# Performance work log

Hardware: AMD Instinct MI355X
Metric: run time of the kernel (lower is better)

The kernel has to match this reference:

```python
import jax, jax.numpy as jnp
import numpy as np

C, U, V, D, B = 5, 6144, 6144, 64, 4096  # classes, users, items, feat dim, batch pairs


def setup_inputs() -> dict:
    key = jax.random.key(0)
    ks = jax.random.split(key, 16)
    s = 1.0 / np.sqrt(D)
    adj = (jax.random.uniform(ks[0], (C, U, V)) < 0.01).astype(jnp.float32)
    return {
        "u": jax.random.randint(ks[1], (B,), 0, U),
        "v": jax.random.randint(ks[2], (B,), 0, V),
        "u_emb": jax.random.normal(ks[3], (U, D), jnp.float32) * 0.1,
        "v_emb": jax.random.normal(ks[4], (V, D), jnp.float32) * 0.1,
        "W1u": jax.random.normal(ks[5], (C, D, D), jnp.float32) * s,
        "b1u": jnp.zeros((C, D), jnp.float32),
        "W1v": jax.random.normal(ks[6], (C, D, D), jnp.float32) * s,
        "b1v": jnp.zeros((C, D), jnp.float32),
        "W2u": jax.random.normal(ks[7], (C, D, D), jnp.float32) * s,
        "b2u": jnp.zeros((C, D), jnp.float32),
        "W2v": jax.random.normal(ks[8], (C, D, D), jnp.float32) * s,
        "b2v": jnp.zeros((C, D), jnp.float32),
        "Q": jax.random.normal(ks[9], (C, D, D), jnp.float32) * s,
        "adj": adj,
    }


def reference(u, v, u_emb, v_emb, W1u, b1u, W1v, b1v, W2u, b2u, W2v, b2v, Q, adj):
    # ---- layer 1: per-class graph convolution, summed over rating classes ----
    # user codes aggregate item features through adj_c; item codes through adj_c^T
    msg_v = jnp.einsum("vd,cde->cve", v_emb, W1v)            # [C,V,D]
    h_u = jax.nn.relu(jnp.einsum("cuv,cve->ue", adj, msg_v) + b1v.sum(0))  # [U,D]
    msg_u = jnp.einsum("ud,cde->cue", u_emb, W1u)            # [C,U,D]
    h_v = jax.nn.relu(jnp.einsum("cuv,cue->ve", adj, msg_u) + b1u.sum(0))  # [V,D]
    # ---- layer 2 ----
    z_u = jnp.einsum("cuv,cve->ue", adj, jnp.einsum("vd,cde->cve", h_v, W2u)) + b2u.sum(0)
    z_v = jnp.einsum("cuv,cue->ve", adj, jnp.einsum("ud,cde->cue", h_u, W2v)) + b2v.sum(0)
    # ---- bilinear decoder over batch of (user, item) pairs ----
    zu = z_u[u]                                              # [B,D] gather
    zv = z_v[v]                                              # [B,D] gather
    logits = jnp.einsum("bd,cde,be->bc", zu, Q, zv)          # [B,C] per-class rating logits
    return logits
```

## Files before the change

kernel.cpp:

```cpp
#include <hip/hip_runtime.h>

#define NC   5
#define NU   6144
#define NV   6144
#define ND   64
#define NB   4096
#define CAP  128
#define HALF (NC * NU)

__device__ __forceinline__ unsigned int spread4(unsigned int x) {
  x &= 0xFFu;
  x = (x | (x << 12)) & 0x000F000Fu;
  x = (x | (x << 6))  & 0x03030303u;
  x = (x | (x << 3))  & 0x11111111u;
  return x;
}

__global__ __launch_bounds__(256) void k_adj2idx(
    const float* __restrict__ adj,
    int* __restrict__ cnt,
    unsigned short* __restrict__ idx) {
  __shared__ unsigned int rowwords[64][9];
  const int x = blockIdx.x & 7;
  const int s = blockIdx.x >> 3;
  const int tv = s % 24;
  const int S = (s / 24) * 8 + x;
  const int c  = S / 96;
  const int tu = S - c * 96;
  const int wave = threadIdx.x >> 6;
  const int lane = threadIdx.x & 63;

  float4 av[16];
  {
    const float* base = adj +
        ((size_t)(c * NU + tu * 64 + wave * 16) * NV + tv * 256);
    #pragma unroll
    for (int rr = 0; rr < 16; ++rr)
      av[rr] = ((const float4*)(base + (size_t)rr * NV))[lane];
  }
  #pragma unroll
  for (int rr = 0; rr < 16; ++rr) {
    const unsigned long long b0 = __ballot(av[rr].x != 0.0f);
    const unsigned long long b1 = __ballot(av[rr].y != 0.0f);
    const unsigned long long b2 = __ballot(av[rr].z != 0.0f);
    const unsigned long long b3 = __ballot(av[rr].w != 0.0f);
    if (lane < 8) {
      const unsigned int e0 = spread4((unsigned int)(b0 >> (lane * 8)));
      const unsigned int e1 = spread4((unsigned int)(b1 >> (lane * 8)));
      const unsigned int e2 = spread4((unsigned int)(b2 >> (lane * 8)));
      const unsigned int e3 = spread4((unsigned int)(b3 >> (lane * 8)));
      rowwords[wave * 16 + rr][lane] = e0 | (e1 << 1) | (e2 << 2) | (e3 << 3);
    }
  }
  __syncthreads();

  #pragma unroll
  for (int p = 0; p < 2; ++p) {
    const int rloc = lane >> 3;
    const int wloc = lane & 7;
    const int r = wave * 16 + p * 8 + rloc;
    const unsigned int wbits = rowwords[r][wloc];
    const int pc = __popc(wbits);
    int pre = pc;
    #pragma unroll
    for (int d = 1; d < 8; d <<= 1) {
      const int y = __shfl_up(pre, d, 64);
      if (wloc >= d) pre += y;
    }
    const int total = __shfl(pre, rloc * 8 + 7, 64);
    const int excl  = pre - pc;
    const int R = c * 6144 + tu * 64 + r;
    int base = 0;
    if (wloc == 0 && total > 0) base = atomicAdd(&cnt[R], total);
    base = __shfl(base, rloc * 8, 64);
    unsigned int m = wbits;
    int o = base + excl;
    unsigned short* orow = idx + (size_t)R * CAP;
    const int vbase = tv * 256 + wloc * 32;
    while (m) {
      const int bb = __ffs(m) - 1;
      if (o < CAP) orow[o] = (unsigned short)(vbase + bb);
      ++o;
      m &= m - 1;
    }
  }

  {
    const int j = threadIdx.x;
    const int w = j >> 5, bit = j & 31;
    unsigned int w0 = 0, w1 = 0;
    #pragma unroll
    for (int r = 0; r < 32; ++r) {
      w0 |= ((rowwords[r][w]      >> bit) & 1u) << r;
      w1 |= ((rowwords[r + 32][w] >> bit) & 1u) << r;
    }
    const int cj = __popc(w0) + __popc(w1);
    if (cj > 0) {
      const int R = (NC + c) * 6144 + tv * 256 + j;
      int o = atomicAdd(&cnt[R], cj);
      unsigned short* orow = idx + (size_t)R * CAP;
      const int ubase = tu * 64;
      unsigned int m = w0;
      while (m) {
        const int bb = __ffs(m) - 1;
        if (o < CAP) orow[o] = (unsigned short)(ubase + bb);
        ++o;
        m &= m - 1;
      }
      m = w1;
      while (m) {
        const int bb = __ffs(m) - 1;
        if (o < CAP) orow[o] = (unsigned short)(ubase + 32 + bb);
        ++o;
        m &= m - 1;
      }
    }
  }
}

__global__ __launch_bounds__(256) void k_layer(
    const int* __restrict__ cnt,
    const unsigned short* __restrict__ idx,
    const float* __restrict__ tabA,
    const float* __restrict__ tabB,
    const float* __restrict__ Wa, const float* __restrict__ ba,
    float* __restrict__ outA,
    const float* __restrict__ Wb, const float* __restrict__ bb,
    float* __restrict__ outB,
    int do_relu) {
  __shared__ float4 lds_agg[NC][16][16];
  const int side = blockIdx.x >= 384;
  const int r0   = (blockIdx.x - side * 384) * 16;
  const float4* tab = (const float4*)(side ? tabB : tabA);
  const float* W    = side ? Wb : Wa;
  const float* bias = side ? bb : ba;
  float* out        = side ? outB : outA;
  const int wave = threadIdx.x >> 6;
  const int lane = threadIdx.x & 63;
  const int g    = lane >> 4;
  const int e16  = lane & 15;

  for (int rr = wave * 4; rr < wave * 4 + 4; ++rr) {
    for (int c = 0; c < NC; ++c) {
      const int R = side * HALF + c * 6144 + r0 + rr;
      int n = cnt[R];
      n = n > CAP ? CAP : n;
      const unsigned short* l = idx + (size_t)R * CAP;
      float4 a0 = make_float4(0.f,0.f,0.f,0.f), a1 = a0, a2 = a0, a3 = a0;
      int i = 0;
      for (; i + 16 <= n; i += 16) {
        const int j0 = l[i + g], j1 = l[i + 4 + g];
        const int j2 = l[i + 8 + g], j3 = l[i + 12 + g];
        const float4 x0 = tab[j0 * 16 + e16];
        const float4 x1 = tab[j1 * 16 + e16];
        const float4 x2 = tab[j2 * 16 + e16];
        const float4 x3 = tab[j3 * 16 + e16];
        a0.x += x0.x; a0.y += x0.y; a0.z += x0.z; a0.w += x0.w;
        a1.x += x1.x; a1.y += x1.y; a1.z += x1.z; a1.w += x1.w;
        a2.x += x2.x; a2.y += x2.y; a2.z += x2.z; a2.w += x2.w;
        a3.x += x3.x; a3.y += x3.y; a3.z += x3.z; a3.w += x3.w;
      }
      for (; i + 4 <= n; i += 4) {
        const float4 x = tab[(int)l[i + g] * 16 + e16];
        a0.x += x.x; a0.y += x.y; a0.z += x.z; a0.w += x.w;
      }
      if (i + g < n) {
        const float4 x = tab[(int)l[i + g] * 16 + e16];
        a1.x += x.x; a1.y += x.y; a1.z += x.z; a1.w += x.w;
      }
      a0.x += a1.x + a2.x + a3.x;
      a0.y += a1.y + a2.y + a3.y;
      a0.z += a1.z + a2.z + a3.z;
      a0.w += a1.w + a2.w + a3.w;
      #pragma unroll
      for (int off = 16; off < 64; off <<= 1) {
        a0.x += __shfl_xor(a0.x, off, 64);
        a0.y += __shfl_xor(a0.y, off, 64);
        a0.z += __shfl_xor(a0.z, off, 64);
        a0.w += __shfl_xor(a0.w, off, 64);
      }
      if (g == 0) lds_agg[c][rr][e16] = a0;
    }
  }
  __syncthreads();

  float bs = 0.0f;
  #pragma unroll
  for (int c = 0; c < NC; ++c) bs += bias[c * 64 + lane];
  float acc[4] = {bs, bs, bs, bs};
  for (int c = 0; c < NC; ++c) {
    float w[64];
    #pragma unroll
    for (int d = 0; d < 64; ++d) w[d] = W[c * 4096 + d * 64 + lane];
    #pragma unroll
    for (int r = 0; r < 4; ++r) {
      #pragma unroll
      for (int d4 = 0; d4 < 16; ++d4) {
        const float4 a = lds_agg[c][wave * 4 + r][d4];
        acc[r] = fmaf(a.x, w[d4 * 4 + 0], acc[r]);
        acc[r] = fmaf(a.y, w[d4 * 4 + 1], acc[r]);
        acc[r] = fmaf(a.z, w[d4 * 4 + 2], acc[r]);
        acc[r] = fmaf(a.w, w[d4 * 4 + 3], acc[r]);
      }
    }
  }
  #pragma unroll
  for (int r = 0; r < 4; ++r) {
    const float v = do_relu ? fmaxf(acc[r], 0.0f) : acc[r];
    out[(size_t)(r0 + wave * 4 + r) * 64 + lane] = v;
  }
}

__global__ __launch_bounds__(256) void k_decoder(
    const int* __restrict__ uu, const int* __restrict__ vv,
    const float* __restrict__ z_u, const float* __restrict__ z_v,
    const float* __restrict__ Q,
    float* __restrict__ out) {
  const int lane = threadIdx.x & 63;
  const int wave = threadIdx.x >> 6;
  const int b = blockIdx.x * 4 + wave;
  const int ub = uu[b];
  const int vb = vv[b];
  const float zve = z_v[(size_t)vb * 64 + lane];
  const float* zu = z_u + (size_t)ub * 64;
  #pragma unroll
  for (int c = 0; c < NC; ++c) {
    const float* Qc = Q + c * 64 * 64;
    float t = 0.0f;
    #pragma unroll
    for (int d = 0; d < 64; ++d) t = fmaf(zu[d], Qc[d * 64 + lane], t);
    float p = t * zve;
    #pragma unroll
    for (int off = 32; off > 0; off >>= 1) p += __shfl_xor(p, off, 64);
    if (lane == 0) out[(size_t)b * NC + c] = p;
  }
}

extern "C" void kernel_launch(void* const* d_in, const int* in_sizes, int n_in,
                              void* d_out, int out_size, void* d_ws, size_t ws_size,
                              hipStream_t stream) {
  const int*   u     = (const int*)d_in[0];
  const int*   v     = (const int*)d_in[1];
  const float* u_emb = (const float*)d_in[2];
  const float* v_emb = (const float*)d_in[3];
  const float* W1u   = (const float*)d_in[4];
  const float* b1u   = (const float*)d_in[5];
  const float* W1v   = (const float*)d_in[6];
  const float* b1v   = (const float*)d_in[7];
  const float* W2u   = (const float*)d_in[8];
  const float* b2u   = (const float*)d_in[9];
  const float* W2v   = (const float*)d_in[10];
  const float* b2v   = (const float*)d_in[11];
  const float* Q     = (const float*)d_in[12];
  const float* adj   = (const float*)d_in[13];
  float* out = (float*)d_out;

  char* ws = (char*)d_ws;
  int* cnt = (int*)ws;
  unsigned short* idxL = (unsigned short*)(ws + 245760);
  char* fbase = ws + 245760 + 15728640;
  float* h_u = (float*)fbase;
  float* h_v = (float*)(fbase + 1572864);
  float* z_u = (float*)(fbase + 3145728);
  float* z_v = (float*)(fbase + 4718592);

  hipMemsetAsync(cnt, 0, 2 * NC * 6144 * sizeof(int), stream);

  k_adj2idx<<<NC * 96 * 24, 256, 0, stream>>>(adj, cnt, idxL);

  k_layer<<<768, 256, 0, stream>>>(cnt, idxL, v_emb, u_emb,
                                   W1v, b1v, h_u, W1u, b1u, h_v, 1);
  k_layer<<<768, 256, 0, stream>>>(cnt, idxL, h_v, h_u,
                                   W2u, b2u, z_u, W2v, b2v, z_v, 0);
  k_decoder<<<NB / 4, 256, 0, stream>>>(u, v, z_u, z_v, Q, out);
}
```

Before: 1.165 ms.

## Enlarge adj-to-index tiles, double-buffer nontemporal loads, register column bitmasks

The adjacency-to-index conversion kernel now processes 256x256 tiles per block instead of 64x256. Each wave streams 64 rows in batches of 8 with register double-buffering and nontemporal loads. Column bitmasks are accumulated in registers rather than transposed from LDS, which cuts the per-column atomics on the transposed side by a factor of four. The cost is more registers per thread and fewer blocks, so less occupancy to hide the latency of the ~750MB adjacency read.

```diff
diff --git a/kernel.cpp b/kernel.cpp
--- a/kernel.cpp
+++ b/kernel.cpp
@@ -8,6 +8,8 @@
 #define CAP  128
 #define HALF (NC * NU)
 
+typedef float vf4 __attribute__((ext_vector_type(4)));
+
 __device__ __forceinline__ unsigned int spread4(unsigned int x) {
   x &= 0xFFu;
   x = (x | (x << 12)) & 0x000F000Fu;
@@ -20,99 +22,121 @@
     const float* __restrict__ adj,
     int* __restrict__ cnt,
     unsigned short* __restrict__ idx) {
-  __shared__ unsigned int rowwords[64][9];
-  const int x = blockIdx.x & 7;
-  const int s = blockIdx.x >> 3;
-  const int tv = s % 24;
-  const int S = (s / 24) * 8 + x;
-  const int c  = S / 96;
-  const int tu = S - c * 96;
+  __shared__ unsigned int rowwords[256][9];
+  __shared__ unsigned int colLDS[256][9];
+  const int b = blockIdx.x;
+  const int c  = b / 576;
+  const int rem = b - c * 576;
+  const int tu = rem / 24;
+  const int tv = rem - tu * 24;
   const int wave = threadIdx.x >> 6;
   const int lane = threadIdx.x & 63;
-
-  float4 av[16];
-  {
-    const float* base = adj +
-        ((size_t)(c * NU + tu * 64 + wave * 16) * NV + tv * 256);
-    #pragma unroll
-    for (int rr = 0; rr < 16; ++rr)
-      av[rr] = ((const float4*)(base + (size_t)rr * NV))[lane];
-  }
-  #pragma unroll
-  for (int rr = 0; rr < 16; ++rr) {
-    const unsigned long long b0 = __ballot(av[rr].x != 0.0f);
-    const unsigned long long b1 = __ballot(av[rr].y != 0.0f);
-    const unsigned long long b2 = __ballot(av[rr].z != 0.0f);
-    const unsigned long long b3 = __ballot(av[rr].w != 0.0f);
-    if (lane < 8) {
-      const unsigned int e0 = spread4((unsigned int)(b0 >> (lane * 8)));
-      const unsigned int e1 = spread4((unsigned int)(b1 >> (lane * 8)));
-      const unsigned int e2 = spread4((unsigned int)(b2 >> (lane * 8)));
-      const unsigned int e3 = spread4((unsigned int)(b3 >> (lane * 8)));
-      rowwords[wave * 16 + rr][lane] = e0 | (e1 << 1) | (e2 << 2) | (e3 << 3);
-    }
+  const int R0 = wave * 64;
+
+  unsigned int cacc[8];
+  #pragma unroll
+  for (int k = 0; k < 8; ++k) cacc[k] = 0;
+
+  const float* wbase = adj +
+      ((size_t)(c * NU + tu * 256 + R0) * NV + tv * 256);
+
+  vf4 av[8];
+  #pragma unroll
+  for (int rr = 0; rr < 8; ++rr)
+    av[rr] = __builtin_nontemporal_load(
+        (const vf4*)(wbase + (size_t)rr * NV) + lane);
+
+  for (int batch = 0; batch < 8; ++batch) {
+    vf4 nv[8];
+    if (batch < 7) {
+      const float* nb = wbase + (size_t)(batch + 1) * 8 * NV;
+      #pragma unroll
+      for (int rr = 0; rr < 8; ++rr)
+        nv[rr] = __builtin_nontemporal_load(
+            (const vf4*)(nb + (size_t)rr * NV) + lane);
+    }
+
+    #pragma unroll
+    for (int rr = 0; rr < 8; ++rr) {
+      const int r = batch * 8 + rr;
+      const unsigned long long b0 = __ballot(av[rr].x != 0.0f);
+      const unsigned long long b1 = __ballot(av[rr].y != 0.0f);
+      const unsigned long long b2 = __ballot(av[rr].z != 0.0f);
+      const unsigned long long b3 = __ballot(av[rr].w != 0.0f);
+      if (lane < 8) {
+        const unsigned int e0 = spread4((unsigned int)(b0 >> (lane * 8)));
+        const unsigned int e1 = spread4((unsigned int)(b1 >> (lane * 8)));
+        const unsigned int e2 = spread4((unsigned int)(b2 >> (lane * 8)));
+        const unsigned int e3 = spread4((unsigned int)(b3 >> (lane * 8)));
+        rowwords[R0 + r][lane] = e0 | (e1 << 1) | (e2 << 2) | (e3 << 3);
+      }
+      const unsigned int bit = 1u << (r & 31);
+      const int h = r >> 5;
+      if (av[rr].x != 0.0f) cacc[0 + h] |= bit;
+      if (av[rr].y != 0.0f) cacc[2 + h] |= bit;
+      if (av[rr].z != 0.0f) cacc[4 + h] |= bit;
+      if (av[rr].w != 0.0f) cacc[6 + h] |= bit;
+    }
+    __threadfence_block();
+
+    {
+      const int rloc = lane >> 3;
+      const int wloc = lane & 7;
+      const unsigned int wbits = rowwords[R0 + batch * 8 + rloc][wloc];
+      const int pc = __popc(wbits);
+      int pre = pc;
+      #pragma unroll
+      for (int d = 1; d < 8; d <<= 1) {
+        const int y = __shfl_up(pre, d, 64);
+        if (wloc >= d) pre += y;
+      }
+      const int total = __shfl(pre, rloc * 8 + 7, 64);
+      const int excl  = pre - pc;
+      const int R = c * 6144 + tu * 256 + R0 + batch * 8 + rloc;
+      int base = 0;
+      if (wloc == 0 && total > 0) base = atomicAdd(&cnt[R], total);
+      base = __shfl(base, rloc * 8, 64);
+      unsigned int m = wbits;
+      int o = base + excl;
+      unsigned short* orow = idx + (size_t)R * CAP;
+      const int vbase = tv * 256 + wloc * 32;
+      while (m) {
+        const int bb = __ffs(m) - 1;
+        if (o < CAP) orow[o] = (unsigned short)(vbase + bb);
+        ++o;
+        m &= m - 1;
+      }
+    }
+    #pragma unroll
+    for (int rr = 0; rr < 8; ++rr) av[rr] = nv[rr];
+  }
+
+  #pragma unroll
+  for (int k = 0; k < 4; ++k) {
+    colLDS[lane * 4 + k][wave * 2 + 0] = cacc[k * 2 + 0];
+    colLDS[lane * 4 + k][wave * 2 + 1] = cacc[k * 2 + 1];
   }
   __syncthreads();
-
-  #pragma unroll
-  for (int p = 0; p < 2; ++p) {
-    const int rloc = lane >> 3;
-    const int wloc = lane & 7;
-    const int r = wave * 16 + p * 8 + rloc;
-    const unsigned int wbits = rowwords[r][wloc];
-    const int pc = __popc(wbits);
-    int pre = pc;
-    #pragma unroll
-    for (int d = 1; d < 8; d <<= 1) {
-      const int y = __shfl_up(pre, d, 64);
-      if (wloc >= d) pre += y;
-    }
-    const int total = __shfl(pre, rloc * 8 + 7, 64);
-    const int excl  = pre - pc;
-    const int R = c * 6144 + tu * 64 + r;
-    int base = 0;
-    if (wloc == 0 && total > 0) base = atomicAdd(&cnt[R], total);
-    base = __shfl(base, rloc * 8, 64);
-    unsigned int m = wbits;
-    int o = base + excl;
-    unsigned short* orow = idx + (size_t)R * CAP;
-    const int vbase = tv * 256 + wloc * 32;
-    while (m) {
-      const int bb = __ffs(m) - 1;
-      if (o < CAP) orow[o] = (unsigned short)(vbase + bb);
-      ++o;
-      m &= m - 1;
-    }
-  }
-
   {
     const int j = threadIdx.x;
-    const int w = j >> 5, bit = j & 31;
-    unsigned int w0 = 0, w1 = 0;
-    #pragma unroll
-    for (int r = 0; r < 32; ++r) {
-      w0 |= ((rowwords[r][w]      >> bit) & 1u) << r;
-      w1 |= ((rowwords[r + 32][w] >> bit) & 1u) << r;
-    }
-    const int cj = __popc(w0) + __popc(w1);
-    if (cj > 0) {
+    unsigned int m8[8];
+    int tot = 0;
+    #pragma unroll
+    for (int w = 0; w < 8; ++w) { m8[w] = colLDS[j][w]; tot += __popc(m8[w]); }
+    if (tot > 0) {
       const int R = (NC + c) * 6144 + tv * 256 + j;
-      int o = atomicAdd(&cnt[R], cj);
+      int o = atomicAdd(&cnt[R], tot);
       unsigned short* orow = idx + (size_t)R * CAP;
-      const int ubase = tu * 64;
-      unsigned int m = w0;
-      while (m) {
-        const int bb = __ffs(m) - 1;
-        if (o < CAP) orow[o] = (unsigned short)(ubase + bb);
-        ++o;
-        m &= m - 1;
-      }
-      m = w1;
-      while (m) {
-        const int bb = __ffs(m) - 1;
-        if (o < CAP) orow[o] = (unsigned short)(ubase + 32 + bb);
-        ++o;
-        m &= m - 1;
+      #pragma unroll
+      for (int w = 0; w < 8; ++w) {
+        unsigned int m = m8[w];
+        const int ub = tu * 256 + (w >> 1) * 64 + (w & 1) * 32;
+        while (m) {
+          const int bb = __ffs(m) - 1;
+          if (o < CAP) orow[o] = (unsigned short)(ub + bb);
+          ++o;
+          m &= m - 1;
+        }
       }
     }
   }
@@ -264,9 +288,9 @@
   float* z_u = (float*)(fbase + 3145728);
   float* z_v = (float*)(fbase + 4718592);
 
-  hipMemsetAsync(cnt, 0, 2 * NC * 6144 * sizeof(int), stream);
-
-  k_adj2idx<<<NC * 96 * 24, 256, 0, stream>>>(adj, cnt, idxL);
+  (void)hipMemsetAsync(cnt, 0, 2 * NC * 6144 * sizeof(int), stream);
+
+  k_adj2idx<<<NC * 24 * 24, 256, 0, stream>>>(adj, cnt, idxL);
 
   k_layer<<<768, 256, 0, stream>>>(cnt, idxL, v_emb, u_emb,
                                    W1v, b1v, h_u, W1u, b1u, h_v, 1);
```

New measurement: 1.185 ms. About the same (+1.8%).
